# Optimization experiments

Measured on AMD Instinct MI355X. Metric: run time of the kernel, lower is better.

## Reference

```python
import jax, jax.numpy as jnp
import numpy as np

T_DATA, E_NO, I_NO, SUB_NO = 10000, 2000, 500, 64
KERN_LEN, PAD = 201, 100


def setup_inputs() -> dict:
    key = jax.random.key(0)
    ks = jax.random.split(key, 8)
    S_e = (jax.random.uniform(ks[0], (T_DATA, E_NO)) < 0.05).astype(jnp.float32)
    S_i = (jax.random.uniform(ks[1], (T_DATA, I_NO)) < 0.05).astype(jnp.float32)
    # Synapse->subunit assignment: each synapse feeds exactly one subunit (one-hot rows of C_syn.T)
    ae = jax.random.randint(ks[2], (E_NO,), 0, SUB_NO)
    ai = jax.random.randint(ks[3], (I_NO,), 0, SUB_NO)
    C_syn_e = jax.nn.one_hot(ae, SUB_NO, dtype=jnp.float32).T  # [sub_no, E_no]
    C_syn_i = jax.nn.one_hot(ai, SUB_NO, dtype=jnp.float32).T  # [sub_no, I_no]
    # Sparse dendritic coupling matrix (binary tree-like connectivity)
    C_den = (jax.random.uniform(ks[4], (SUB_NO, SUB_NO)) < 0.05).astype(jnp.float32)
    # Learned raw parameters (per __init__: ones * init)
    weight_raw = jnp.zeros((SUB_NO, 2), jnp.float32)          # weight_init = 0.0
    decay_raw = jnp.full((SUB_NO,), 2.0, jnp.float32)         # decay_init = 2.0
    threshold_raw = jnp.zeros((SUB_NO,), jnp.float32)         # threshold_init = 0.0
    prop_raw = jnp.full((SUB_NO,), -1.0, jnp.float32)         # prop_init = -1.0
    return {"S_e": S_e, "S_i": S_i, "C_den": C_den, "C_syn_e": C_syn_e,
            "C_syn_i": C_syn_i, "weight_raw": weight_raw, "decay_raw": decay_raw,
            "threshold_raw": threshold_raw, "prop_raw": prop_raw}


def reference(S_e, S_i, C_den, C_syn_e, C_syn_i, weight_raw, decay_raw, threshold_raw, prop_raw):
    sub_no = C_den.shape[0]
    # Project presynaptic spikes onto subunits: [T, sub_no]
    syn_e = S_e @ C_syn_e.T
    syn_i = S_i @ C_syn_i.T
    weight_e = jnp.exp(weight_raw[:, 0])
    weight_i = -jnp.exp(weight_raw[:, 1])
    decay = jax.nn.sigmoid(decay_raw)
    threshold = -jnp.exp(threshold_raw)
    prop = jnpp = jnp.exp(prop_raw)
    drive = syn_e * weight_e[None, :] + syn_i * weight_i[None, :]  # [T, sub_no]

    def step_fn(carry, d_t):
        V, spk = carry
        # reset-on-spike, leak, synaptic drive, dendritic propagation of spikes
        V = V * (1.0 - spk) * decay + d_t + (spk * prop) @ C_den.T
        spk = jnp.heaviside(V + threshold, jnp.float32(0.0))
        return (V, spk), spk

    init = (jnp.zeros(sub_no, jnp.float32), jnp.zeros(sub_no, jnp.float32))
    _, spk_out = jax.lax.scan(step_fn, init, drive)  # spk_out: [T, sub_no]

    # Alpha-kernel smoothing of root subunit spike train (Tau, W are fixed buffers)
    t_tau = jnp.arange(KERN_LEN, dtype=jnp.float32) / jnp.exp(jnp.float32(2.0))
    kern = t_tau * jnp.exp(-t_tau) * jnp.exp(jnp.float32(0.75))
    kern_flipped = jnp.flip(kern)
    x = spk_out[:, 0][None, None, :]               # [1,1,T]
    w = kern_flipped[None, None, :]                # [1,1,201]
    final = jax.lax.conv_general_dilated(x, w, (1,), [(PAD, PAD)]).reshape(-1)
    return final, spk_out
```

## Files before the change

### kernel.cpp

```cpp
#include <hip/hip_runtime.h>
#include <math.h>

#define T_DATA 10000
#define E_NO 2000
#define I_NO 500
#define SUB_NO 64
#define KERN_LEN 201
#define PAD 100
#define NBLK 314
typedef unsigned long long ull;

__global__ void assign_kernel(const float* __restrict__ Ce, const float* __restrict__ Ci,
                              int* __restrict__ ae, int* __restrict__ ai) {
    int idx = blockIdx.x * 256 + threadIdx.x;
    if (idx < E_NO) {
        int a = 0;
        for (int s = 0; s < SUB_NO; ++s)
            if (Ce[(size_t)s * E_NO + idx] != 0.0f) a = s;
        ae[idx] = a;
    } else if (idx < E_NO + I_NO) {
        int i = idx - E_NO;
        int a = 0;
        for (int s = 0; s < SUB_NO; ++s)
            if (Ci[(size_t)s * I_NO + i] != 0.0f) a = s;
        ai[i] = a;
    }
}

__global__ void drive_kernel(const float* __restrict__ Se, const float* __restrict__ Si,
                             const float* __restrict__ wraw,
                             const int* __restrict__ ae, const int* __restrict__ ai,
                             float* __restrict__ drive) {
    __shared__ float be[SUB_NO];
    __shared__ float bi[SUB_NO];
    int t = blockIdx.x;
    int tid = threadIdx.x;
    if (tid < SUB_NO) { be[tid] = 0.0f; bi[tid] = 0.0f; }
    __syncthreads();
    const float4* se4 = (const float4*)(Se + (size_t)t * E_NO);
    for (int e4 = tid; e4 < E_NO / 4; e4 += 256) {
        float4 v = se4[e4];
        int b = e4 * 4;
        if (v.x != 0.0f) atomicAdd(&be[ae[b + 0]], 1.0f);
        if (v.y != 0.0f) atomicAdd(&be[ae[b + 1]], 1.0f);
        if (v.z != 0.0f) atomicAdd(&be[ae[b + 2]], 1.0f);
        if (v.w != 0.0f) atomicAdd(&be[ae[b + 3]], 1.0f);
    }
    const float4* si4 = (const float4*)(Si + (size_t)t * I_NO);
    for (int i4 = tid; i4 < I_NO / 4; i4 += 256) {
        float4 v = si4[i4];
        int b = i4 * 4;
        if (v.x != 0.0f) atomicAdd(&bi[ai[b + 0]], 1.0f);
        if (v.y != 0.0f) atomicAdd(&bi[ai[b + 1]], 1.0f);
        if (v.z != 0.0f) atomicAdd(&bi[ai[b + 2]], 1.0f);
        if (v.w != 0.0f) atomicAdd(&bi[ai[b + 3]], 1.0f);
    }
    __syncthreads();
    if (tid < SUB_NO) {
        float we = (float)exp((double)wraw[2 * tid]);
        float wi = -(float)exp((double)wraw[2 * tid + 1]);
        drive[(size_t)t * SUB_NO + tid] =
            __fadd_rn(__fmul_rn(be[tid], we), __fmul_rn(bi[tid], wi));
    }
}


#define SL(B,NB,OFF,LIT,BITS) \
  "v_and_b32 v16, vcc_lo, %[rlo]\n\t" \
  "v_and_b32 v17, vcc_hi, %[rhi]\n\t" \
  "v_cndmask_b32 v21, v29, " B ", vcc\n\t" \
  "v_bcnt_u32_b32 v18, v16, 0\n\t" \
  "v_bcnt_u32_b32 v18, v17, v18\n\t" \
  "v_cvt_f32_u32 v19, v18\n\t" \
  "global_load_dword " B ", v[24:25], off offset:" OFF "\n\t" \
  "v_mul_f32 v20, v19, %[p]\n\t" \
  "v_add_f32 v28, v21, v20\n\t" \
  "v_cmp_gt_f32 vcc, v28, %[thr]\n\t" \
  "v_mul_f32 v29, v28, %[dec]\n\t" \
  "v_or_b32 v22, " LIT ", " BITS "\n\t" \
  "v_cndmask_b32 " BITS ", " BITS ", v22, vcc\n\t" \
  "s_waitcnt vmcnt(31)\n\t" \
  "v_add_f32 v29, v29, " NB "\n\t"

#define SL0(B,NB,OFF,BITS) \
  "v_and_b32 v16, vcc_lo, %[rlo]\n\t" \
  "v_and_b32 v17, vcc_hi, %[rhi]\n\t" \
  "v_cndmask_b32 v21, v29, " B ", vcc\n\t" \
  "v_bcnt_u32_b32 v18, v16, 0\n\t" \
  "v_bcnt_u32_b32 v18, v17, v18\n\t" \
  "v_cvt_f32_u32 v19, v18\n\t" \
  "global_load_dword " B ", v[24:25], off offset:" OFF "\n\t" \
  "v_mul_f32 v20, v19, %[p]\n\t" \
  "v_add_f32 v28, v21, v20\n\t" \
  "v_cmp_gt_f32 vcc, v28, %[thr]\n\t" \
  "v_mul_f32 v29, v28, %[dec]\n\t" \
  "v_cndmask_b32 " BITS ", 0, 1, vcc\n\t" \
  "s_waitcnt vmcnt(31)\n\t" \
  "v_add_f32 v29, v29, " NB "\n\t"

#define SB(B,NB,OFF,LIT,BITS) \
  "v_and_b32 v16, vcc_lo, %[rlo]\n\t" \
  "v_and_b32 v17, vcc_hi, %[rhi]\n\t" \
  "v_cndmask_b32 v21, v29, " B ", vcc\n\t" \
  "v_bcnt_u32_b32 v18, v16, 0\n\t" \
  "v_bcnt_u32_b32 v18, v17, v18\n\t" \
  "v_lshlrev_b32 v18, 2, v18\n\t" \
  "ds_bpermute_b32 v20, v18, %[vt]\n\t" \
  "global_load_dword " B ", v[24:25], off offset:" OFF "\n\t" \
  "s_waitcnt lgkmcnt(0)\n\t" \
  "v_add_f32 v28, v21, v20\n\t" \
  "v_cmp_gt_f32 vcc, v28, %[thr]\n\t" \
  "v_mul_f32 v29, v28, %[dec]\n\t" \
  "v_or_b32 v22, " LIT ", " BITS "\n\t" \
  "v_cndmask_b32 " BITS ", " BITS ", v22, vcc\n\t" \
  "s_waitcnt vmcnt(31)\n\t" \
  "v_add_f32 v29, v29, " NB "\n\t"

#define SB0(B,NB,OFF,BITS) \
  "v_and_b32 v16, vcc_lo, %[rlo]\n\t" \
  "v_and_b32 v17, vcc_hi, %[rhi]\n\t" \
  "v_cndmask_b32 v21, v29, " B ", vcc\n\t" \
  "v_bcnt_u32_b32 v18, v16, 0\n\t" \
  "v_bcnt_u32_b32 v18, v17, v18\n\t" \
  "v_lshlrev_b32 v18, 2, v18\n\t" \
  "ds_bpermute_b32 v20, v18, %[vt]\n\t" \
  "global_load_dword " B ", v[24:25], off offset:" OFF "\n\t" \
  "s_waitcnt lgkmcnt(0)\n\t" \
  "v_add_f32 v28, v21, v20\n\t" \
  "v_cmp_gt_f32 vcc, v28, %[thr]\n\t" \
  "v_mul_f32 v29, v28, %[dec]\n\t" \
  "v_cndmask_b32 " BITS ", 0, 1, vcc\n\t" \
  "s_waitcnt vmcnt(31)\n\t" \
  "v_add_f32 v29, v29, " NB "\n\t"

#define BUMPL "v_add_u32 v24, s16, v24\n\t"
#define STOREW(BITS) \
  "global_store_dword v[26:27], " BITS ", off\n\t" \
  "v_add_u32 v26, s17, v26\n\t"

#define BLK(S,S0,BITS) \
  S0("v32","v33","0",BITS) \
  S("v33","v34","256","2",BITS)          S("v34","v35","512","4",BITS) \
  S("v35","v36","768","8",BITS)          S("v36","v37","1024","16",BITS) \
  S("v37","v38","1280","32",BITS)        S("v38","v39","1536","64",BITS) \
  S("v39","v40","1792","0x80",BITS)      S("v40","v41","2048","0x100",BITS) \
  S("v41","v42","2304","0x200",BITS)     S("v42","v43","2560","0x400",BITS) \
  S("v43","v44","2816","0x800",BITS)     S("v44","v45","3072","0x1000",BITS) \
  S("v45","v46","3328","0x2000",BITS)    S("v46","v47","3584","0x4000",BITS) \
  S("v47","v48","3840","0x8000",BITS) \
  BUMPL \
  S("v48","v49","0","0x10000",BITS)      S("v49","v50","256","0x20000",BITS) \
  S("v50","v51","512","0x40000",BITS)    S("v51","v52","768","0x80000",BITS) \
  S("v52","v53","1024","0x100000",BITS)  S("v53","v54","1280","0x200000",BITS) \
  S("v54","v55","1536","0x400000",BITS)  S("v55","v56","1792","0x800000",BITS) \
  S("v56","v57","2048","0x1000000",BITS) S("v57","v58","2304","0x2000000",BITS) \
  S("v58","v59","2560","0x4000000",BITS) S("v59","v60","2816","0x8000000",BITS) \
  S("v60","v61","3072","0x10000000",BITS) S("v61","v62","3328","0x20000000",BITS) \
  S("v62","v63","3584","0x40000000",BITS) S("v63","v32","3840","0x80000000",BITS) \
  BUMPL

#define PRO \
  "v_mov_b32 v24, %[alo]\n\t" "v_mov_b32 v25, %[ahi]\n\t" \
  "v_mov_b32 v26, %[blo]\n\t" "v_mov_b32 v27, %[bhi]\n\t" \
  "s_mov_b32 s16, 0x1000\n\t" "s_mov_b32 s17, 0x100\n\t" \
  "global_load_dword v32, v[24:25], off offset:0\n\t" \
  "global_load_dword v33, v[24:25], off offset:256\n\t" \
  "global_load_dword v34, v[24:25], off offset:512\n\t" \
  "global_load_dword v35, v[24:25], off offset:768\n\t" \
  "global_load_dword v36, v[24:25], off offset:1024\n\t" \
  "global_load_dword v37, v[24:25], off offset:1280\n\t" \
  "global_load_dword v38, v[24:25], off offset:1536\n\t" \
  "global_load_dword v39, v[24:25], off offset:1792\n\t" \
  "global_load_dword v40, v[24:25], off offset:2048\n\t" \
  "global_load_dword v41, v[24:25], off offset:2304\n\t" \
  "global_load_dword v42, v[24:25], off offset:2560\n\t" \
  "global_load_dword v43, v[24:25], off offset:2816\n\t" \
  "global_load_dword v44, v[24:25], off offset:3072\n\t" \
  "global_load_dword v45, v[24:25], off offset:3328\n\t" \
  "global_load_dword v46, v[24:25], off offset:3584\n\t" \
  "global_load_dword v47, v[24:25], off offset:3840\n\t" \
  BUMPL \
  "global_load_dword v48, v[24:25], off offset:0\n\t" \
  "global_load_dword v49, v[24:25], off offset:256\n\t" \
  "global_load_dword v50, v[24:25], off offset:512\n\t" \
  "global_load_dword v51, v[24:25], off offset:768\n\t" \
  "global_load_dword v52, v[24:25], off offset:1024\n\t" \
  "global_load_dword v53, v[24:25], off offset:1280\n\t" \
  "global_load_dword v54, v[24:25], off offset:1536\n\t" \
  "global_load_dword v55, v[24:25], off offset:1792\n\t" \
  "global_load_dword v56, v[24:25], off offset:2048\n\t" \
  "global_load_dword v57, v[24:25], off offset:2304\n\t" \
  "global_load_dword v58, v[24:25], off offset:2560\n\t" \
  "global_load_dword v59, v[24:25], off offset:2816\n\t" \
  "global_load_dword v60, v[24:25], off offset:3072\n\t" \
  "global_load_dword v61, v[24:25], off offset:3328\n\t" \
  "global_load_dword v62, v[24:25], off offset:3584\n\t" \
  "global_load_dword v63, v[24:25], off offset:3840\n\t" \
  BUMPL \
  "s_mov_b64 vcc, 0\n\t" \
  "s_nop 2\n\t" \
  "s_movk_i32 s20, 157\n\t" \
  "s_waitcnt vmcnt(31)\n\t" \
  "v_mov_b32 v29, v32\n\t" \
  "v_mov_b32 v28, 0\n\t"

#define CLOBBERS \
  "v16","v17","v18","v19","v20","v21","v22","v23","v24","v25","v26","v27", \
  "v28","v29","v30","v31","v32","v33","v34","v35","v36","v37","v38","v39", \
  "v40","v41","v42","v43","v44","v45","v46","v47","v48","v49","v50","v51", \
  "v52","v53","v54","v55","v56","v57","v58","v59","v60","v61","v62","v63", \
  "s16","s17","s20","vcc","scc","memory"

__device__ void scan_lin_hot(const float* drive, unsigned* packed,
                             unsigned rlo, unsigned rhi, float p, float dec,
                             float thr, int s) {
    ull a = (ull)drive + (ull)s * 4;
    ull b = (ull)packed + (ull)s * 4;
    asm volatile(
        PRO
        "Lmain%=:\n\t"
        BLK(SL, SL0, "v23") STOREW("v23")
        BLK(SL, SL0, "v30") STOREW("v30")
        "s_add_i32 s20, s20, -1\n\t"
        "s_cmp_lg_u32 s20, 0\n\t"
        "s_cbranch_scc1 Lmain%=\n\t"
        :
        : [alo]"v"((unsigned)a), [ahi]"v"((unsigned)(a >> 32)),
          [blo]"v"((unsigned)b), [bhi]"v"((unsigned)(b >> 32)),
          [rlo]"v"(rlo), [rhi]"v"(rhi), [p]"v"(p), [dec]"v"(dec), [thr]"v"(thr)
        : CLOBBERS);
}

__device__ void scan_bp_hot(const float* drive, unsigned* packed,
                            unsigned rlo, unsigned rhi, float dec,
                            float thr, float vtab, int s) {
    ull a = (ull)drive + (ull)s * 4;
    ull b = (ull)packed + (ull)s * 4;
    asm volatile(
        PRO
        "Lmainb%=:\n\t"
        BLK(SB, SB0, "v23") STOREW("v23")
        BLK(SB, SB0, "v30") STOREW("v30")
        "s_add_i32 s20, s20, -1\n\t"
        "s_cmp_lg_u32 s20, 0\n\t"
        "s_cbranch_scc1 Lmainb%=\n\t"
        :
        : [alo]"v"((unsigned)a), [ahi]"v"((unsigned)(a >> 32)),
          [blo]"v"((unsigned)b), [bhi]"v"((unsigned)(b >> 32)),
          [rlo]"v"(rlo), [rhi]"v"(rhi), [vt]"v"(vtab), [dec]"v"(dec), [thr]"v"(thr)
        : CLOBBERS);
}

#define C_LIN(DK, DK1, LIT) \
  "v_and_b32 %[tlo], vcc_lo, %[crlo]\n\t" \
  "v_and_b32 %[thi], vcc_hi, %[crhi]\n\t" \
  "v_cndmask_b32 %[base], %[w0], %[" DK "], vcc\n\t" \
  "v_bcnt_u32_b32 %[kc], %[tlo], 0\n\t" \
  "v_bcnt_u32_b32 %[kc], %[thi], %[kc]\n\t" \
  "v_cvt_f32_u32 %[kf], %[kc]\n\t" \
  "v_mul_f32 %[acc], %[kf], %[cp]\n\t" \
  "v_add_f32 %[vv], %[base], %[acc]\n\t" \
  "v_cmp_gt_f32 vcc, %[vv], %[cthr]\n\t" \
  "v_mul_f32 %[w0], %[vv], %[cdec]\n\t" \
  "v_add_f32 %[w0], %[w0], %[" DK1 "]\n\t" \
  "v_or_b32 %[tmp], " LIT ", %[bits]\n\t" \
  "v_cndmask_b32 %[bits], %[bits], %[tmp], vcc\n\t"

#define CSTEPS32 \
  C_LIN("d0","d1","1")            C_LIN("d1","d2","2")            C_LIN("d2","d3","4")            C_LIN("d3","d4","8") \
  C_LIN("d4","d5","16")           C_LIN("d5","d6","32")           C_LIN("d6","d7","64")           C_LIN("d7","d8","0x80") \
  C_LIN("d8","d9","0x100")        C_LIN("d9","d10","0x200")       C_LIN("d10","d11","0x400")      C_LIN("d11","d12","0x800") \
  C_LIN("d12","d13","0x1000")     C_LIN("d13","d14","0x2000")     C_LIN("d14","d15","0x4000")     C_LIN("d15","d16","0x8000") \
  C_LIN("d16","d17","0x10000")    C_LIN("d17","d18","0x20000")    C_LIN("d18","d19","0x40000")    C_LIN("d19","d20","0x80000") \
  C_LIN("d20","d21","0x100000")   C_LIN("d21","d22","0x200000")   C_LIN("d22","d23","0x400000")   C_LIN("d23","d24","0x800000") \
  C_LIN("d24","d25","0x1000000")  C_LIN("d25","d26","0x2000000")  C_LIN("d26","d27","0x4000000")  C_LIN("d27","d28","0x8000000") \
  C_LIN("d28","d29","0x10000000") C_LIN("d29","d30","0x20000000") C_LIN("d30","d31","0x40000000") C_LIN("d31","d32","0x80000000")

#define CRUN_BLOCK(B) do { \
    unsigned _tlo, _thi, _kc, _tmp, _bits; float _kf, _acc, _base; \
    ull _mout; \
    asm volatile( \
        "s_mov_b64 vcc, %[min]\n\t" \
        "v_mov_b32 %[bits], 0\n\t" \
        "s_nop 1\n\t" \
        CSTEPS32 \
        "s_mov_b64 %[mout], vcc\n\t" \
        : [vv]"+v"(V), [w0]"+v"(w0), [bits]"=&v"(_bits), [mout]"=s"(_mout), \
          [tlo]"=&v"(_tlo), [thi]"=&v"(_thi), [kc]"=&v"(_kc), [tmp]"=&v"(_tmp), \
          [kf]"=&v"(_kf), [acc]"=&v"(_acc), [base]"=&v"(_base) \
        : [min]"s"(m), [crlo]"v"(row_lo), [crhi]"v"(row_hi), [cp]"v"(p0), \
          [cdec]"v"(decay), [cthr]"v"(thrpos), \
          [d0]"v"(B[0]),  [d1]"v"(B[1]),  [d2]"v"(B[2]),  [d3]"v"(B[3]), \
          [d4]"v"(B[4]),  [d5]"v"(B[5]),  [d6]"v"(B[6]),  [d7]"v"(B[7]), \
          [d8]"v"(B[8]),  [d9]"v"(B[9]),  [d10]"v"(B[10]), [d11]"v"(B[11]), \
          [d12]"v"(B[12]), [d13]"v"(B[13]), [d14]"v"(B[14]), [d15]"v"(B[15]), \
          [d16]"v"(B[16]), [d17]"v"(B[17]), [d18]"v"(B[18]), [d19]"v"(B[19]), \
          [d20]"v"(B[20]), [d21]"v"(B[21]), [d22]"v"(B[22]), [d23]"v"(B[23]), \
          [d24]"v"(B[24]), [d25]"v"(B[25]), [d26]"v"(B[26]), [d27]"v"(B[27]), \
          [d28]"v"(B[28]), [d29]"v"(B[29]), [d30]"v"(B[30]), [d31]"v"(B[31]), \
          [d32]"v"(B[32]) \
        : "vcc"); \
    m = _mout; bitsv = _bits; } while (0)

__device__ void scan_lin_c(const float* drive, unsigned* packed,
                           unsigned row_lo, unsigned row_hi, float p0,
                           float decay, float thrpos, int s) {
    const float* dp = drive + s;
    unsigned* pw = packed + s;
    float bufA[33], bufB[33];
#pragma unroll
    for (int k = 0; k < 33; ++k) bufA[k] = dp[(size_t)k * SUB_NO];
    float V = 0.0f, w0 = bufA[0];
    ull m = 0ull;
    unsigned bitsv;
    for (int b = 0; b < NBLK; b += 2) {
#pragma unroll
        for (int k = 0; k < 33; ++k) bufB[k] = dp[((size_t)(b + 1) * 32 + k) * SUB_NO];
        CRUN_BLOCK(bufA);
        pw[(size_t)b * SUB_NO] = bitsv;
#pragma unroll
        for (int k = 0; k < 33; ++k) bufA[k] = dp[((size_t)(b + 2) * 32 + k) * SUB_NO];
        CRUN_BLOCK(bufB);
        pw[(size_t)(b + 1) * SUB_NO] = bitsv;
    }
}

__device__ void scan_slow(const float* drive, unsigned* packed,
                          ull rowmask, const float* prop_l,
                          float decay, float thr, int s) {
    float V = 0.0f;
    bool sp = false;
    ull mask = 0ull;
    for (int b = 0; b < NBLK; ++b) {
        unsigned bits = 0u;
        for (int k = 0; k < 32; ++k) {
            int t = b * 32 + k;
            float d = drive[(size_t)t * SUB_NO + s];
            ull mm = mask & rowmask;
            float acc = 0.0f;
            for (int j = 0; j < SUB_NO; ++j) {
                float c = ((mm >> j) & 1ull) ? prop_l[j] : 0.0f;
                acc = __fadd_rn(acc, c);
            }
            float Vr = sp ? 0.0f : V;
            float bb = __fmul_rn(Vr, decay);
            float cc = __fadd_rn(bb, d);
            V = __fadd_rn(cc, acc);
            float sv = __fadd_rn(V, thr);
            sp = sv > 0.0f;
            mask = __ballot(sp);
            bits |= sp ? (1u << k) : 0u;
        }
        packed[(size_t)b * SUB_NO + s] = bits;
    }
}

__global__ void __launch_bounds__(64, 1)
scan_kernel(const float* drive, const float* __restrict__ Cden,
            const float* __restrict__ decay_raw, const float* __restrict__ thr_raw,
            const float* __restrict__ prop_raw, unsigned* packed, int fast) {
    __shared__ float prop_l[SUB_NO];
    int s = threadIdx.x;
    prop_l[s] = (float)exp((double)prop_raw[s]);
    __syncthreads();
    float myp = prop_l[s];

    float em = (float)exp(-(double)decay_raw[s]);
    float den = __fadd_rn(1.0f, em);
    float decay = (float)(1.0 / (double)den);
    float thrpos = (float)exp((double)thr_raw[s]);
    float thr = -thrpos;

    ull rowmask = 0ull;
    for (int j = 0; j < SUB_NO; ++j)
        if (Cden[(size_t)s * SUB_NO + j] != 0.0f) rowmask |= (1ull << j);
    unsigned row_lo = (unsigned)rowmask;
    unsigned row_hi = (unsigned)(rowmask >> 32);

    float p0 = prop_l[0];
    bool uni = __all(myp == p0);
    int maxk = (int)__popcll(rowmask);
    for (int off = 32; off; off >>= 1) {
        int o = __shfl_xor(maxk, off);
        maxk = maxk > o ? maxk : o;
    }

    float seqk = 0.0f;
    for (int i = 0; i < s; ++i) seqk = __fadd_rn(seqk, p0);
    float vtab = seqk;

    bool lok = (s > maxk) || (seqk == __fmul_rn((float)s, p0));
    bool uselin = uni && __all(lok);

    if (uselin && fast)
        scan_lin_hot(drive, packed, row_lo, row_hi, p0, decay, thrpos, s);
    else if (uselin)
        scan_lin_c(drive, packed, row_lo, row_hi, p0, decay, thrpos, s);
    else if (uni && fast)
        scan_bp_hot(drive, packed, row_lo, row_hi, decay, thrpos, vtab, s);
    else
        scan_slow(drive, packed, rowmask, prop_l, decay, thr, s);
}

__global__ void expand_kernel(const unsigned* __restrict__ packed,
                              float* __restrict__ spk_out) {
    int idx = blockIdx.x * 256 + threadIdx.x;
    int t = idx >> 6, s = idx & 63;
    unsigned w = packed[(size_t)(t >> 5) * SUB_NO + s];
    spk_out[idx] = (float)((w >> (t & 31)) & 1u);
}

__global__ void conv_kernel(const unsigned* __restrict__ packed,
                            float* __restrict__ out) {
    __shared__ float kern_s[KERN_LEN];
    __shared__ float x_s[256 + 2 * PAD];
    int tid = threadIdx.x;
    int t0 = blockIdx.x * 256;

    float e2 = (float)exp(2.0);
    float e075 = (float)exp(0.75);
    for (int m = tid; m < KERN_LEN; m += 256) {
        float tt = (float)m / e2;
        kern_s[m] = __fmul_rn(__fmul_rn(tt, expf(-tt)), e075);
    }
    for (int k = tid; k < 256 + 2 * PAD; k += 256) {
        int idx = t0 - PAD + k;
        float xv = 0.0f;
        if (idx >= 0 && idx < T_DATA) {
            unsigned w = packed[(size_t)(idx >> 5) * SUB_NO];
            xv = (float)((w >> (idx & 31)) & 1u);
        }
        x_s[k] = xv;
    }
    __syncthreads();

    int t = t0 + tid;
    if (t < T_DATA) {
        float acc = 0.0f;
        for (int m = 0; m < KERN_LEN; ++m)
            acc += kern_s[m] * x_s[tid + 2 * PAD - m];
        out[t] = acc;
    }
}

extern "C" void kernel_launch(void* const* d_in, const int* in_sizes, int n_in,
                              void* d_out, int out_size, void* d_ws, size_t ws_size,
                              hipStream_t stream) {
    const float* S_e      = (const float*)d_in[0];
    const float* S_i      = (const float*)d_in[1];
    const float* C_den    = (const float*)d_in[2];
    const float* C_syn_e  = (const float*)d_in[3];
    const float* C_syn_i  = (const float*)d_in[4];
    const float* w_raw    = (const float*)d_in[5];
    const float* dec_raw  = (const float*)d_in[6];
    const float* thr_raw  = (const float*)d_in[7];
    const float* prop_raw = (const float*)d_in[8];

    float* out = (float*)d_out;
    float* ws = (float*)d_ws;
    float* drive = ws;
    int*   ae    = (int*)(ws + 640000);
    int*   ai    = (int*)(ws + 642000);

    size_t need_bytes = (size_t)(642500 + NBLK * SUB_NO) * 4;
    unsigned* packed = (ws_size >= need_bytes)
                           ? (unsigned*)(ws + 642500)
                           : (unsigned*)ws;

    ull da = (ull)drive, pa = (ull)packed;
    int fast = ((da & 0xFFFFFFFFull) + 0x290000ull <= 0x100000000ull) &&
               ((pa & 0xFFFFFFFFull) + 0x30000ull  <= 0x100000000ull) &&
               (ws_size >= need_bytes);

    assign_kernel<<<(E_NO + I_NO + 255) / 256, 256, 0, stream>>>(C_syn_e, C_syn_i, ae, ai);
    drive_kernel<<<T_DATA, 256, 0, stream>>>(S_e, S_i, w_raw, ae, ai, drive);
    scan_kernel<<<256, 64, 0, stream>>>(drive, C_den, dec_raw, thr_raw, prop_raw, packed, fast);
    expand_kernel<<<T_DATA * SUB_NO / 256, 256, 0, stream>>>(packed, out + T_DATA);
    conv_kernel<<<(T_DATA + 255) / 256, 256, 0, stream>>>(packed, out);
}
```

Measured before the change: 557.7 us.

## Transpose drive to time-major per subunit and stream scan with dwordx4 loads

Adds a transpose kernel that writes drive into a per-subunit contiguous layout, staged in the spare tail of the output buffer. The hand-written scan loops now issue 16-byte vector loads with a shallow wait count instead of 32 outstanding scalar strided loads, and the step instructions are reordered for better dual issue. The scan launch shrinks from 256 redundant blocks to one. This adds an extra kernel launch and a transpose pass, and uses the output region as scratch before expand overwrites it.

```diff
diff --git a/kernel.cpp b/kernel.cpp
--- a/kernel.cpp
+++ b/kernel.cpp
@@ -8,6 +8,7 @@
 #define KERN_LEN 201
 #define PAD 100
 #define NBLK 314
+#define TSTRIDE 10112
 typedef unsigned long long ull;
 
 __global__ void assign_kernel(const float* __restrict__ Ce, const float* __restrict__ Ci,
@@ -64,166 +65,176 @@
     }
 }
 
-
-#define SL(B,NB,OFF,LIT,BITS) \
-  "v_and_b32 v16, vcc_lo, %[rlo]\n\t" \
-  "v_and_b32 v17, vcc_hi, %[rhi]\n\t" \
-  "v_cndmask_b32 v21, v29, " B ", vcc\n\t" \
-  "v_bcnt_u32_b32 v18, v16, 0\n\t" \
-  "v_bcnt_u32_b32 v18, v17, v18\n\t" \
-  "v_cvt_f32_u32 v19, v18\n\t" \
-  "global_load_dword " B ", v[24:25], off offset:" OFF "\n\t" \
-  "v_mul_f32 v20, v19, %[p]\n\t" \
-  "v_add_f32 v28, v21, v20\n\t" \
-  "v_cmp_gt_f32 vcc, v28, %[thr]\n\t" \
-  "v_mul_f32 v29, v28, %[dec]\n\t" \
-  "v_or_b32 v22, " LIT ", " BITS "\n\t" \
-  "v_cndmask_b32 " BITS ", " BITS ", v22, vcc\n\t" \
-  "s_waitcnt vmcnt(31)\n\t" \
-  "v_add_f32 v29, v29, " NB "\n\t"
-
-#define SL0(B,NB,OFF,BITS) \
-  "v_and_b32 v16, vcc_lo, %[rlo]\n\t" \
-  "v_and_b32 v17, vcc_hi, %[rhi]\n\t" \
-  "v_cndmask_b32 v21, v29, " B ", vcc\n\t" \
-  "v_bcnt_u32_b32 v18, v16, 0\n\t" \
-  "v_bcnt_u32_b32 v18, v17, v18\n\t" \
-  "v_cvt_f32_u32 v19, v18\n\t" \
-  "global_load_dword " B ", v[24:25], off offset:" OFF "\n\t" \
-  "v_mul_f32 v20, v19, %[p]\n\t" \
-  "v_add_f32 v28, v21, v20\n\t" \
-  "v_cmp_gt_f32 vcc, v28, %[thr]\n\t" \
-  "v_mul_f32 v29, v28, %[dec]\n\t" \
-  "v_cndmask_b32 " BITS ", 0, 1, vcc\n\t" \
-  "s_waitcnt vmcnt(31)\n\t" \
-  "v_add_f32 v29, v29, " NB "\n\t"
-
-#define SB(B,NB,OFF,LIT,BITS) \
-  "v_and_b32 v16, vcc_lo, %[rlo]\n\t" \
-  "v_and_b32 v17, vcc_hi, %[rhi]\n\t" \
-  "v_cndmask_b32 v21, v29, " B ", vcc\n\t" \
-  "v_bcnt_u32_b32 v18, v16, 0\n\t" \
-  "v_bcnt_u32_b32 v18, v17, v18\n\t" \
-  "v_lshlrev_b32 v18, 2, v18\n\t" \
-  "ds_bpermute_b32 v20, v18, %[vt]\n\t" \
-  "global_load_dword " B ", v[24:25], off offset:" OFF "\n\t" \
-  "s_waitcnt lgkmcnt(0)\n\t" \
-  "v_add_f32 v28, v21, v20\n\t" \
-  "v_cmp_gt_f32 vcc, v28, %[thr]\n\t" \
-  "v_mul_f32 v29, v28, %[dec]\n\t" \
-  "v_or_b32 v22, " LIT ", " BITS "\n\t" \
-  "v_cndmask_b32 " BITS ", " BITS ", v22, vcc\n\t" \
-  "s_waitcnt vmcnt(31)\n\t" \
-  "v_add_f32 v29, v29, " NB "\n\t"
-
-#define SB0(B,NB,OFF,BITS) \
-  "v_and_b32 v16, vcc_lo, %[rlo]\n\t" \
-  "v_and_b32 v17, vcc_hi, %[rhi]\n\t" \
-  "v_cndmask_b32 v21, v29, " B ", vcc\n\t" \
-  "v_bcnt_u32_b32 v18, v16, 0\n\t" \
-  "v_bcnt_u32_b32 v18, v17, v18\n\t" \
-  "v_lshlrev_b32 v18, 2, v18\n\t" \
-  "ds_bpermute_b32 v20, v18, %[vt]\n\t" \
-  "global_load_dword " B ", v[24:25], off offset:" OFF "\n\t" \
-  "s_waitcnt lgkmcnt(0)\n\t" \
-  "v_add_f32 v28, v21, v20\n\t" \
-  "v_cmp_gt_f32 vcc, v28, %[thr]\n\t" \
-  "v_mul_f32 v29, v28, %[dec]\n\t" \
-  "v_cndmask_b32 " BITS ", 0, 1, vcc\n\t" \
-  "s_waitcnt vmcnt(31)\n\t" \
-  "v_add_f32 v29, v29, " NB "\n\t"
-
-#define BUMPL "v_add_u32 v24, s16, v24\n\t"
+__global__ void transpose_kernel(const float* __restrict__ drive,
+                                 float* __restrict__ dT) {
+    __shared__ float tile[64][65];
+    int t0 = blockIdx.x * 64;
+    int w = threadIdx.x;
+    for (int k = 0; k < 16; ++k) {
+        int L = w + 256 * k;
+        int i = L >> 6, s = L & 63;
+        int t = t0 + i;
+        tile[i][s] = (t < T_DATA) ? drive[(size_t)t * SUB_NO + s] : 0.0f;
+    }
+    __syncthreads();
+    int l = w & 63, g = w >> 6;
+    for (int k = 0; k < 16; ++k) {
+        int s = g * 16 + k;
+        dT[(size_t)s * TSTRIDE + t0 + l] = tile[l][s];
+    }
+}
+
+
+#define W7 "s_waitcnt vmcnt(7)\n\t"
+#define LOADQ(Q) \
+  "global_load_dwordx4 " Q ", v[24:25], off\n\t" \
+  "v_add_u32 v24, 16, v24\n\t"
 #define STOREW(BITS) \
   "global_store_dword v[26:27], " BITS ", off\n\t" \
   "v_add_u32 v26, s17, v26\n\t"
 
-#define BLK(S,S0,BITS) \
-  S0("v32","v33","0",BITS) \
-  S("v33","v34","256","2",BITS)          S("v34","v35","512","4",BITS) \
-  S("v35","v36","768","8",BITS)          S("v36","v37","1024","16",BITS) \
-  S("v37","v38","1280","32",BITS)        S("v38","v39","1536","64",BITS) \
-  S("v39","v40","1792","0x80",BITS)      S("v40","v41","2048","0x100",BITS) \
-  S("v41","v42","2304","0x200",BITS)     S("v42","v43","2560","0x400",BITS) \
-  S("v43","v44","2816","0x800",BITS)     S("v44","v45","3072","0x1000",BITS) \
-  S("v45","v46","3328","0x2000",BITS)    S("v46","v47","3584","0x4000",BITS) \
-  S("v47","v48","3840","0x8000",BITS) \
-  BUMPL \
-  S("v48","v49","0","0x10000",BITS)      S("v49","v50","256","0x20000",BITS) \
-  S("v50","v51","512","0x40000",BITS)    S("v51","v52","768","0x80000",BITS) \
-  S("v52","v53","1024","0x100000",BITS)  S("v53","v54","1280","0x200000",BITS) \
-  S("v54","v55","1536","0x400000",BITS)  S("v55","v56","1792","0x800000",BITS) \
-  S("v56","v57","2048","0x1000000",BITS) S("v57","v58","2304","0x2000000",BITS) \
-  S("v58","v59","2560","0x4000000",BITS) S("v59","v60","2816","0x8000000",BITS) \
-  S("v60","v61","3072","0x10000000",BITS) S("v61","v62","3328","0x20000000",BITS) \
-  S("v62","v63","3584","0x40000000",BITS) S("v63","v32","3840","0x80000000",BITS) \
-  BUMPL
-
-#define PRO \
+#define QS(D,LIT,BITS) \
+  "v_cmp_gt_f32 vcc, v28, %[thr]\n\t" \
+  "v_mul_f32 v29, v28, %[dec]\n\t" \
+  "v_or_b32 v22, " LIT ", " BITS "\n\t" \
+  "v_and_b32 v16, vcc_lo, %[rlo]\n\t" \
+  "v_and_b32 v17, vcc_hi, %[rhi]\n\t" \
+  "v_add_f32 v29, v29, " D "\n\t" \
+  "v_bcnt_u32_b32 v18, v16, 0\n\t" \
+  "v_bcnt_u32_b32 v18, v17, v18\n\t" \
+  "v_cndmask_b32 v21, v29, " D ", vcc\n\t" \
+  "v_cvt_f32_u32 v19, v18\n\t" \
+  "v_cndmask_b32 " BITS ", " BITS ", v22, vcc\n\t" \
+  "v_mul_f32 v20, v19, %[p]\n\t" \
+  "v_add_f32 v28, v21, v20\n\t"
+
+#define QS0(D,BITS) \
+  "v_cmp_gt_f32 vcc, v28, %[thr]\n\t" \
+  "v_mul_f32 v29, v28, %[dec]\n\t" \
+  "v_and_b32 v16, vcc_lo, %[rlo]\n\t" \
+  "v_and_b32 v17, vcc_hi, %[rhi]\n\t" \
+  "v_add_f32 v29, v29, " D "\n\t" \
+  "v_bcnt_u32_b32 v18, v16, 0\n\t" \
+  "v_bcnt_u32_b32 v18, v17, v18\n\t" \
+  "v_cndmask_b32 v21, v29, " D ", vcc\n\t" \
+  "v_cvt_f32_u32 v19, v18\n\t" \
+  "v_cndmask_b32 " BITS ", 0, 1, vcc\n\t" \
+  "v_mul_f32 v20, v19, %[p]\n\t" \
+  "v_add_f32 v28, v21, v20\n\t"
+
+#define QSP(D) \
+  "v_cmp_gt_f32 vcc, v28, %[thr]\n\t" \
+  "v_mul_f32 v29, v28, %[dec]\n\t" \
+  "v_and_b32 v16, vcc_lo, %[rlo]\n\t" \
+  "v_and_b32 v17, vcc_hi, %[rhi]\n\t" \
+  "v_add_f32 v29, v29, " D "\n\t" \
+  "v_bcnt_u32_b32 v18, v16, 0\n\t" \
+  "v_bcnt_u32_b32 v18, v17, v18\n\t" \
+  "v_cndmask_b32 v21, v29, " D ", vcc\n\t" \
+  "v_cvt_f32_u32 v19, v18\n\t" \
+  "v_mul_f32 v20, v19, %[p]\n\t" \
+  "v_add_f32 v28, v21, v20\n\t"
+
+#define GRP(BITS) \
+  W7 QS0("v33",BITS) QS("v34","2",BITS) QS("v35","4",BITS) LOADQ("v[32:35]") \
+  W7 QS("v36","8",BITS) QS("v37","16",BITS) QS("v38","32",BITS) QS("v39","64",BITS) LOADQ("v[36:39]") \
+  W7 QS("v40","0x80",BITS) QS("v41","0x100",BITS) QS("v42","0x200",BITS) QS("v43","0x400",BITS) LOADQ("v[40:43]") \
+  W7 QS("v44","0x800",BITS) QS("v45","0x1000",BITS) QS("v46","0x2000",BITS) QS("v47","0x4000",BITS) LOADQ("v[44:47]") \
+  W7 QS("v48","0x8000",BITS) QS("v49","0x10000",BITS) QS("v50","0x20000",BITS) QS("v51","0x40000",BITS) LOADQ("v[48:51]") \
+  W7 QS("v52","0x80000",BITS) QS("v53","0x100000",BITS) QS("v54","0x200000",BITS) QS("v55","0x400000",BITS) LOADQ("v[52:55]") \
+  W7 QS("v56","0x800000",BITS) QS("v57","0x1000000",BITS) QS("v58","0x2000000",BITS) QS("v59","0x4000000",BITS) LOADQ("v[56:59]") \
+  W7 QS("v60","0x8000000",BITS) QS("v61","0x10000000",BITS) QS("v62","0x20000000",BITS) QS("v63","0x40000000",BITS) LOADQ("v[60:63]") \
+  W7 QS("v32","0x80000000",BITS) \
+  STOREW(BITS)
+
+#define QSB(D,LIT,BITS) \
+  "v_cmp_gt_f32 vcc, v28, %[thr]\n\t" \
+  "v_or_b32 v22, " LIT ", " BITS "\n\t" \
+  "v_mul_f32 v29, v28, %[dec]\n\t" \
+  "v_and_b32 v16, vcc_lo, %[rlo]\n\t" \
+  "v_and_b32 v17, vcc_hi, %[rhi]\n\t" \
+  "v_add_f32 v29, v29, " D "\n\t" \
+  "v_bcnt_u32_b32 v18, v16, 0\n\t" \
+  "v_bcnt_u32_b32 v18, v17, v18\n\t" \
+  "v_lshlrev_b32 v18, 2, v18\n\t" \
+  "ds_bpermute_b32 v20, v18, %[vt]\n\t" \
+  "v_cndmask_b32 v21, v29, " D ", vcc\n\t" \
+  "v_cndmask_b32 " BITS ", " BITS ", v22, vcc\n\t" \
+  "s_waitcnt lgkmcnt(0)\n\t" \
+  "v_add_f32 v28, v21, v20\n\t"
+
+#define QSB0(D,BITS) \
+  "v_cmp_gt_f32 vcc, v28, %[thr]\n\t" \
+  "v_mul_f32 v29, v28, %[dec]\n\t" \
+  "v_and_b32 v16, vcc_lo, %[rlo]\n\t" \
+  "v_and_b32 v17, vcc_hi, %[rhi]\n\t" \
+  "v_add_f32 v29, v29, " D "\n\t" \
+  "v_bcnt_u32_b32 v18, v16, 0\n\t" \
+  "v_bcnt_u32_b32 v18, v17, v18\n\t" \
+  "v_lshlrev_b32 v18, 2, v18\n\t" \
+  "ds_bpermute_b32 v20, v18, %[vt]\n\t" \
+  "v_cndmask_b32 v21, v29, " D ", vcc\n\t" \
+  "v_cndmask_b32 " BITS ", 0, 1, vcc\n\t" \
+  "s_waitcnt lgkmcnt(0)\n\t" \
+  "v_add_f32 v28, v21, v20\n\t"
+
+#define QSBP(D) \
+  "v_cmp_gt_f32 vcc, v28, %[thr]\n\t" \
+  "v_mul_f32 v29, v28, %[dec]\n\t" \
+  "v_and_b32 v16, vcc_lo, %[rlo]\n\t" \
+  "v_and_b32 v17, vcc_hi, %[rhi]\n\t" \
+  "v_add_f32 v29, v29, " D "\n\t" \
+  "v_bcnt_u32_b32 v18, v16, 0\n\t" \
+  "v_bcnt_u32_b32 v18, v17, v18\n\t" \
+  "v_lshlrev_b32 v18, 2, v18\n\t" \
+  "ds_bpermute_b32 v20, v18, %[vt]\n\t" \
+  "v_cndmask_b32 v21, v29, " D ", vcc\n\t" \
+  "s_waitcnt lgkmcnt(0)\n\t" \
+  "v_add_f32 v28, v21, v20\n\t"
+
+#define GRPB(BITS) \
+  W7 QSB0("v33",BITS) QSB("v34","2",BITS) QSB("v35","4",BITS) LOADQ("v[32:35]") \
+  W7 QSB("v36","8",BITS) QSB("v37","16",BITS) QSB("v38","32",BITS) QSB("v39","64",BITS) LOADQ("v[36:39]") \
+  W7 QSB("v40","0x80",BITS) QSB("v41","0x100",BITS) QSB("v42","0x200",BITS) QSB("v43","0x400",BITS) LOADQ("v[40:43]") \
+  W7 QSB("v44","0x800",BITS) QSB("v45","0x1000",BITS) QSB("v46","0x2000",BITS) QSB("v47","0x4000",BITS) LOADQ("v[44:47]") \
+  W7 QSB("v48","0x8000",BITS) QSB("v49","0x10000",BITS) QSB("v50","0x20000",BITS) QSB("v51","0x40000",BITS) LOADQ("v[48:51]") \
+  W7 QSB("v52","0x80000",BITS) QSB("v53","0x100000",BITS) QSB("v54","0x200000",BITS) QSB("v55","0x400000",BITS) LOADQ("v[52:55]") \
+  W7 QSB("v56","0x800000",BITS) QSB("v57","0x1000000",BITS) QSB("v58","0x2000000",BITS) QSB("v59","0x4000000",BITS) LOADQ("v[56:59]") \
+  W7 QSB("v60","0x8000000",BITS) QSB("v61","0x10000000",BITS) QSB("v62","0x20000000",BITS) QSB("v63","0x40000000",BITS) LOADQ("v[60:63]") \
+  W7 QSB("v32","0x80000000",BITS) \
+  STOREW(BITS)
+
+#define VPRO \
   "v_mov_b32 v24, %[alo]\n\t" "v_mov_b32 v25, %[ahi]\n\t" \
   "v_mov_b32 v26, %[blo]\n\t" "v_mov_b32 v27, %[bhi]\n\t" \
-  "s_mov_b32 s16, 0x1000\n\t" "s_mov_b32 s17, 0x100\n\t" \
-  "global_load_dword v32, v[24:25], off offset:0\n\t" \
-  "global_load_dword v33, v[24:25], off offset:256\n\t" \
-  "global_load_dword v34, v[24:25], off offset:512\n\t" \
-  "global_load_dword v35, v[24:25], off offset:768\n\t" \
-  "global_load_dword v36, v[24:25], off offset:1024\n\t" \
-  "global_load_dword v37, v[24:25], off offset:1280\n\t" \
-  "global_load_dword v38, v[24:25], off offset:1536\n\t" \
-  "global_load_dword v39, v[24:25], off offset:1792\n\t" \
-  "global_load_dword v40, v[24:25], off offset:2048\n\t" \
-  "global_load_dword v41, v[24:25], off offset:2304\n\t" \
-  "global_load_dword v42, v[24:25], off offset:2560\n\t" \
-  "global_load_dword v43, v[24:25], off offset:2816\n\t" \
-  "global_load_dword v44, v[24:25], off offset:3072\n\t" \
-  "global_load_dword v45, v[24:25], off offset:3328\n\t" \
-  "global_load_dword v46, v[24:25], off offset:3584\n\t" \
-  "global_load_dword v47, v[24:25], off offset:3840\n\t" \
-  BUMPL \
-  "global_load_dword v48, v[24:25], off offset:0\n\t" \
-  "global_load_dword v49, v[24:25], off offset:256\n\t" \
-  "global_load_dword v50, v[24:25], off offset:512\n\t" \
-  "global_load_dword v51, v[24:25], off offset:768\n\t" \
-  "global_load_dword v52, v[24:25], off offset:1024\n\t" \
-  "global_load_dword v53, v[24:25], off offset:1280\n\t" \
-  "global_load_dword v54, v[24:25], off offset:1536\n\t" \
-  "global_load_dword v55, v[24:25], off offset:1792\n\t" \
-  "global_load_dword v56, v[24:25], off offset:2048\n\t" \
-  "global_load_dword v57, v[24:25], off offset:2304\n\t" \
-  "global_load_dword v58, v[24:25], off offset:2560\n\t" \
-  "global_load_dword v59, v[24:25], off offset:2816\n\t" \
-  "global_load_dword v60, v[24:25], off offset:3072\n\t" \
-  "global_load_dword v61, v[24:25], off offset:3328\n\t" \
-  "global_load_dword v62, v[24:25], off offset:3584\n\t" \
-  "global_load_dword v63, v[24:25], off offset:3840\n\t" \
-  BUMPL \
-  "s_mov_b64 vcc, 0\n\t" \
-  "s_nop 2\n\t" \
+  "s_mov_b32 s17, 0x100\n\t" \
+  LOADQ("v[32:35]") LOADQ("v[36:39]") LOADQ("v[40:43]") LOADQ("v[44:47]") \
+  LOADQ("v[48:51]") LOADQ("v[52:55]") LOADQ("v[56:59]") LOADQ("v[60:63]") \
   "s_movk_i32 s20, 157\n\t" \
-  "s_waitcnt vmcnt(31)\n\t" \
-  "v_mov_b32 v29, v32\n\t" \
-  "v_mov_b32 v28, 0\n\t"
+  "v_mov_b32 v28, 0\n\t" \
+  W7
 
 #define CLOBBERS \
   "v16","v17","v18","v19","v20","v21","v22","v23","v24","v25","v26","v27", \
   "v28","v29","v30","v31","v32","v33","v34","v35","v36","v37","v38","v39", \
   "v40","v41","v42","v43","v44","v45","v46","v47","v48","v49","v50","v51", \
   "v52","v53","v54","v55","v56","v57","v58","v59","v60","v61","v62","v63", \
-  "s16","s17","s20","vcc","scc","memory"
-
-__device__ void scan_lin_hot(const float* drive, unsigned* packed,
-                             unsigned rlo, unsigned rhi, float p, float dec,
-                             float thr, int s) {
-    ull a = (ull)drive + (ull)s * 4;
+  "s17","s20","vcc","scc","memory"
+
+__device__ void scan_linT_hot(const float* dT, unsigned* packed,
+                              unsigned rlo, unsigned rhi, float p, float dec,
+                              float thr, int s) {
+    ull a = (ull)dT + (ull)s * (TSTRIDE * 4);
     ull b = (ull)packed + (ull)s * 4;
     asm volatile(
-        PRO
-        "Lmain%=:\n\t"
-        BLK(SL, SL0, "v23") STOREW("v23")
-        BLK(SL, SL0, "v30") STOREW("v30")
+        VPRO
+        QSP("v32")
+        "Lt%=:\n\t"
+        GRP("v23")
+        GRP("v30")
         "s_add_i32 s20, s20, -1\n\t"
         "s_cmp_lg_u32 s20, 0\n\t"
-        "s_cbranch_scc1 Lmain%=\n\t"
+        "s_cbranch_scc1 Lt%=\n\t"
         :
         : [alo]"v"((unsigned)a), [ahi]"v"((unsigned)(a >> 32)),
           [blo]"v"((unsigned)b), [bhi]"v"((unsigned)(b >> 32)),
@@ -231,19 +242,20 @@
         : CLOBBERS);
 }
 
-__device__ void scan_bp_hot(const float* drive, unsigned* packed,
-                            unsigned rlo, unsigned rhi, float dec,
-                            float thr, float vtab, int s) {
-    ull a = (ull)drive + (ull)s * 4;
+__device__ void scan_bpT_hot(const float* dT, unsigned* packed,
+                             unsigned rlo, unsigned rhi, float dec,
+                             float thr, float vtab, int s) {
+    ull a = (ull)dT + (ull)s * (TSTRIDE * 4);
     ull b = (ull)packed + (ull)s * 4;
     asm volatile(
-        PRO
-        "Lmainb%=:\n\t"
-        BLK(SB, SB0, "v23") STOREW("v23")
-        BLK(SB, SB0, "v30") STOREW("v30")
+        VPRO
+        QSBP("v32")
+        "Lu%=:\n\t"
+        GRPB("v23")
+        GRPB("v30")
         "s_add_i32 s20, s20, -1\n\t"
         "s_cmp_lg_u32 s20, 0\n\t"
-        "s_cbranch_scc1 Lmainb%=\n\t"
+        "s_cbranch_scc1 Lu%=\n\t"
         :
         : [alo]"v"((unsigned)a), [ahi]"v"((unsigned)(a >> 32)),
           [blo]"v"((unsigned)b), [bhi]"v"((unsigned)(b >> 32)),
@@ -356,7 +368,7 @@
 }
 
 __global__ void __launch_bounds__(64, 1)
-scan_kernel(const float* drive, const float* __restrict__ Cden,
+scan_kernel(const float* drive, const float* dT, const float* __restrict__ Cden,
             const float* __restrict__ decay_raw, const float* __restrict__ thr_raw,
             const float* __restrict__ prop_raw, unsigned* packed, int fast) {
     __shared__ float prop_l[SUB_NO];
@@ -393,11 +405,11 @@
     bool uselin = uni && __all(lok);
 
     if (uselin && fast)
-        scan_lin_hot(drive, packed, row_lo, row_hi, p0, decay, thrpos, s);
+        scan_linT_hot(dT, packed, row_lo, row_hi, p0, decay, thrpos, s);
+    else if (uni && fast)
+        scan_bpT_hot(dT, packed, row_lo, row_hi, decay, thrpos, vtab, s);
     else if (uselin)
         scan_lin_c(drive, packed, row_lo, row_hi, p0, decay, thrpos, s);
-    else if (uni && fast)
-        scan_bp_hot(drive, packed, row_lo, row_hi, decay, thrpos, vtab, s);
     else
         scan_slow(drive, packed, rowmask, prop_l, decay, thr, s);
 }
@@ -467,14 +479,17 @@
                            ? (unsigned*)(ws + 642500)
                            : (unsigned*)ws;
 
-    ull da = (ull)drive, pa = (ull)packed;
-    int fast = ((da & 0xFFFFFFFFull) + 0x290000ull <= 0x100000000ull) &&
+    float* dT = out + (650000 - 64 * TSTRIDE);
+
+    ull ta = (ull)dT, pa = (ull)packed;
+    int fast = ((ta & 0xFFFFFFFFull) + 0x280000ull <= 0x100000000ull) &&
                ((pa & 0xFFFFFFFFull) + 0x30000ull  <= 0x100000000ull) &&
                (ws_size >= need_bytes);
 
     assign_kernel<<<(E_NO + I_NO + 255) / 256, 256, 0, stream>>>(C_syn_e, C_syn_i, ae, ai);
     drive_kernel<<<T_DATA, 256, 0, stream>>>(S_e, S_i, w_raw, ae, ai, drive);
-    scan_kernel<<<256, 64, 0, stream>>>(drive, C_den, dec_raw, thr_raw, prop_raw, packed, fast);
+    transpose_kernel<<<158, 256, 0, stream>>>(drive, dT);
+    scan_kernel<<<1, 64, 0, stream>>>(drive, dT, C_den, dec_raw, thr_raw, prop_raw, packed, fast);
     expand_kernel<<<T_DATA * SUB_NO / 256, 256, 0, stream>>>(packed, out + T_DATA);
     conv_kernel<<<(T_DATA + 255) / 256, 256, 0, stream>>>(packed, out);
 }
```

After: 527.1 us. -5.5%, faster.
